# Performance work log

Measured on AMD Instinct MI355X. Metric: run time of the kernel, lower is better.

## Reference

```python
import jax, jax.numpy as jnp
import numpy as np
import math

N_HEAD = 12


def setup_inputs() -> dict:
    key = jax.random.key(0)
    ks = jax.random.split(key, 4)
    B, T, C = 8, 1024, 768
    s = 0.02
    return {
        "x": jax.random.normal(ks[0], (B, T, C), dtype=jnp.float32),
        "attn_mask": jnp.ones((B, T), dtype=jnp.int32),
        "W_attn": jax.random.normal(ks[1], (C, 3 * C), dtype=jnp.float32) * s,
        "b_attn": jnp.zeros((3 * C,), dtype=jnp.float32),
        "W_proj": jax.random.normal(ks[2], (C, C), dtype=jnp.float32) * s,
        "b_proj": jnp.zeros((C,), dtype=jnp.float32),
    }


def reference(x, attn_mask, W_attn, b_attn, W_proj, b_proj):
    B, T, C = x.shape
    hd = C // N_HEAD
    qkv = x @ W_attn + b_attn                      # [B, T, 3C]
    q, k, v = jnp.split(qkv, 3, axis=2)
    # [B, H, T, hd]
    q = q.reshape(B, T, N_HEAD, hd).transpose(0, 2, 1, 3)
    k = k.reshape(B, T, N_HEAD, hd).transpose(0, 2, 1, 3)
    v = v.reshape(B, T, N_HEAD, hd).transpose(0, 2, 1, 3)
    scores = jnp.einsum("bhqd,bhkd->bhqk", q, k) * (1.0 / math.sqrt(hd))
    mask = attn_mask[:, None, None, :]             # [B, 1, 1, T] broadcast over H, q
    scores = jnp.where(mask == 0, -jnp.inf, scores)
    attn = jax.nn.softmax(scores, axis=-1)
    out = jnp.einsum("bhqk,bhkd->bhqd", attn, v)   # [B, H, T, hd]
    out = out.transpose(0, 2, 1, 3).reshape(B, T, C)
    return out @ W_proj + b_proj
```

## Files before the change

### kernel.cpp

```cpp
#include <hip/hip_runtime.h>
#include <hip/hip_bf16.h>
#include <math.h>

constexpr int Bsz  = 8;
constexpr int Tseq = 1024;
constexpr int Cdim = 768;
constexpr int NH   = 12;
constexpr int HD   = 64;
constexpr int Mrows = Bsz * Tseq;
constexpr int C3    = 3 * Cdim;

using short8  = __attribute__((ext_vector_type(8))) short;
using s4v     = __attribute__((ext_vector_type(4))) short;
using floatx4 = __attribute__((ext_vector_type(4))) float;

__device__ __forceinline__ unsigned short f32_to_bf16_rn(float f) {
    unsigned int u = __float_as_uint(f);
    unsigned int r = u + 0x7FFFu + ((u >> 16) & 1u);
    return (unsigned short)(r >> 16);
}
__device__ __forceinline__ unsigned pack_bf16x2_rn(float a, float b) {
    float2 f2; f2.x = a; f2.y = b;
    __hip_bfloat162 h = __float22bfloat162_rn(f2);
    unsigned r;
    __builtin_memcpy(&r, &h, sizeof(r));
    return r;
}
__device__ __forceinline__ short8 lds_ld8(const unsigned short* p) {
    s4v a = *(const s4v*)p;
    s4v b = *(const s4v*)(p + 4);
    return __builtin_shufflevector(a, b, 0, 1, 2, 3, 4, 5, 6, 7);
}
__device__ __forceinline__ void lds_st8(unsigned short* p, short8 v) {
    *(s4v*)p       = __builtin_shufflevector(v, v, 0, 1, 2, 3);
    *(s4v*)(p + 4) = __builtin_shufflevector(v, v, 4, 5, 6, 7);
}

#define GLOAD_LDS16(g, l) __builtin_amdgcn_global_load_lds(                    \
    (const __attribute__((address_space(1))) void*)(g),                        \
    (__attribute__((address_space(3))) void*)(l), 16, 0, 0)

#define WAITVM0 asm volatile("s_waitcnt vmcnt(0)" ::: "memory")
#define LDS_XLANE_FENCE do {                                                   \
    asm volatile("s_waitcnt lgkmcnt(0)" ::: "memory");                         \
    __builtin_amdgcn_sched_barrier(0);                                         \
} while (0)

__global__ __launch_bounds__(256)
void to_bf16(const float* __restrict__ in, unsigned short* __restrict__ out, int n4)
{
    int t = blockIdx.x * blockDim.x + threadIdx.x;
    if (t >= n4) return;
    float4 v = ((const float4*)in)[t];
    ushort4 o;
    o.x = f32_to_bf16_rn(v.x);
    o.y = f32_to_bf16_rn(v.y);
    o.z = f32_to_bf16_rn(v.z);
    o.w = f32_to_bf16_rn(v.w);
    ((ushort4*)out)[t] = o;
}

__global__ __launch_bounds__(256)
void transpose_bf16(const float* __restrict__ in, unsigned short* __restrict__ out,
                    int K, int N)
{
    __shared__ float tile[32][33];
    const int k0 = blockIdx.y * 32, n0 = blockIdx.x * 32;
    const int tx = threadIdx.x & 31, ty = threadIdx.x >> 5;
    #pragma unroll
    for (int r = ty; r < 32; r += 8)
        tile[r][tx] = in[(size_t)(k0 + r) * N + n0 + tx];
    __syncthreads();
    #pragma unroll
    for (int r = ty; r < 32; r += 8)
        out[(size_t)(n0 + r) * K + k0 + tx] = f32_to_bf16_rn(tile[tx][r]);
}

template<int MH>
__device__ __forceinline__ void qkv_body(
    const unsigned short* __restrict__ A_g,
    const unsigned short* __restrict__ B_g,
    const float* __restrict__ bias,
    unsigned short* __restrict__ Cb,
    const int row0, const int col0, const int K, const int N,
    unsigned short* lds)
{
    constexpr int BK   = 32;
    constexpr int BUFS = 16384;

    const int tid  = threadIdx.x;
    const int wave = tid >> 6;
    const int lane = tid & 63;
    const int lm   = lane & 15;
    const int quad = lane >> 4;
    const int wy   = wave >> 2;
    const int wx   = wave & 3;
    const int NI   = K / BK;
    const int sq8  = (quad ^ ((lm ^ (lm >> 2)) & 3)) * 8;
    const int sr   = tid >> 2;
    const int sq   = tid & 3;

    floatx4 acc[4 * MH][4] = {};

    auto stageA = [&](int buf, int k0, int h) {
        const int r  = h * 128 + sr;
        const int gc = k0 + ((sq ^ ((r ^ (r >> 2)) & 3)) << 3);
        GLOAD_LDS16(A_g + (size_t)(row0 + r) * K + gc,
                    lds + buf * BUFS + r * 32 + sq * 8);
    };
    auto stageB = [&](int buf, int k0, int h) {
        const int r  = h * 128 + sr;
        const int gc = k0 + ((sq ^ ((r ^ (r >> 2)) & 3)) << 3);
        GLOAD_LDS16(B_g + (size_t)(col0 + r) * K + gc,
                    lds + buf * BUFS + 8192 + r * 32 + sq * 8);
    };

    #pragma unroll
    for (int h = 0; h < MH; ++h) stageA(0, 0, h);
    stageB(0, 0, 0); stageB(0, 0, 1);
    #pragma unroll
    for (int h = 0; h < MH; ++h) stageA(1, BK, h);
    stageB(1, BK, 0); stageB(1, BK, 1);
    if constexpr (MH == 2) asm volatile("s_waitcnt vmcnt(4)" ::: "memory");
    else                   asm volatile("s_waitcnt vmcnt(3)" ::: "memory");
    __builtin_amdgcn_s_barrier();

    short8 af[2 * MH], bf[4];
    int cur = 0;
    for (int kt = 0; kt < NI; ++kt) {
        const unsigned short* bufA = lds + cur * BUFS;
        const unsigned short* bufB = bufA + 8192;
        const int  stg  = (cur + 2 >= 3) ? cur - 1 : cur + 2;
        const int  k2   = (kt + 2) * BK;
        const bool doSt = (kt + 2 < NI);

        #pragma unroll
        for (int u = 0; u < 2 * MH; ++u)
            af[u] = *(const short8*)(bufA + (wy * (64 * MH) + u * 16 + lm) * 32 + sq8);
        #pragma unroll
        for (int j = 0; j < 4; ++j)
            bf[j] = *(const short8*)(bufB + (wx * 64 + j * 16 + lm) * 32 + sq8);
        if (doSt) {
            stageA(stg, k2, 0);
            if constexpr (MH == 2) stageA(stg, k2, 1); else stageB(stg, k2, 0);
        }
        __builtin_amdgcn_s_barrier();
        __builtin_amdgcn_s_setprio(1);
        #pragma unroll
        for (int u = 0; u < 2 * MH; ++u)
            #pragma unroll
            for (int j = 0; j < 4; ++j)
                acc[u][j] = __builtin_amdgcn_mfma_f32_16x16x32_bf16(af[u], bf[j], acc[u][j], 0, 0, 0);
        __builtin_amdgcn_s_setprio(0);
        __builtin_amdgcn_s_barrier();

        #pragma unroll
        for (int u = 0; u < 2 * MH; ++u)
            af[u] = *(const short8*)(bufA + (wy * (64 * MH) + (2 * MH + u) * 16 + lm) * 32 + sq8);
        if (doSt) {
            if constexpr (MH == 2) { stageB(stg, k2, 0); stageB(stg, k2, 1); }
            else                   stageB(stg, k2, 1);
        }
        __builtin_amdgcn_s_barrier();
        __builtin_amdgcn_s_setprio(1);
        #pragma unroll
        for (int u = 0; u < 2 * MH; ++u)
            #pragma unroll
            for (int j = 0; j < 4; ++j)
                acc[2 * MH + u][j] = __builtin_amdgcn_mfma_f32_16x16x32_bf16(af[u], bf[j], acc[2 * MH + u][j], 0, 0, 0);
        __builtin_amdgcn_s_setprio(0);
        if (kt == NI - 2) { WAITVM0; }
        else if (kt < NI - 2) {
            if constexpr (MH == 2) asm volatile("s_waitcnt vmcnt(4)" ::: "memory");
            else                   asm volatile("s_waitcnt vmcnt(3)" ::: "memory");
        }
        __builtin_amdgcn_s_barrier();

        cur = (cur == 2) ? 0 : cur + 1;
    }
    asm volatile("" ::: "memory");

    unsigned short* wbuf = lds + (NI % 3) * BUFS + wave * 1088;
    float bvj[4];
    #pragma unroll
    for (int j = 0; j < 4; ++j) bvj[j] = bias[col0 + wx * 64 + j * 16 + lm];
    #pragma unroll
    for (int i = 0; i < 4 * MH; ++i) {
        #pragma unroll
        for (int j = 0; j < 4; ++j) {
            #pragma unroll
            for (int r = 0; r < 4; ++r)
                wbuf[(quad * 4 + r) * 68 + j * 16 + lm] = f32_to_bf16_rn(acc[i][j][r] + bvj[j]);
        }
        asm volatile("s_waitcnt lgkmcnt(0)" ::: "memory");
        #pragma unroll
        for (int p = 0; p < 2; ++p) {
            const int lrow  = p * 8 + (lane >> 3);
            const int lcol8 = (lane & 7) * 8;
            short8 v = lds_ld8(&wbuf[lrow * 68 + lcol8]);
            *(short8*)(Cb + (size_t)(row0 + wy * (64 * MH) + i * 16 + lrow) * N +
                       col0 + wx * 64 + lcol8) = v;
        }
        asm volatile("s_waitcnt lgkmcnt(0)" ::: "memory");
    }
}

__global__ __launch_bounds__(512, 1)
void gemm_qkv8p(const unsigned short* __restrict__ A_g,
                const unsigned short* __restrict__ B_g,
                const float* __restrict__ bias,
                unsigned short* __restrict__ Cb)
{
    __shared__ __align__(16) unsigned short lds[3 * 16384];
    const int bid = blockIdx.x;
    if (bid < 256) {
        const int sid = (bid & 7) * 32 + (bid >> 3);
        qkv_body<2>(A_g, B_g, bias, Cb,
                    (sid >> 3) * 256, (sid & 7) * 256, Cdim, C3, lds);
    } else {
        const int t   = bid - 256;
        const int sid = (t & 7) * 8 + (t >> 3);
        qkv_body<1>(A_g, B_g, bias, Cb, sid * 128, 2048, Cdim, C3, lds);
    }
}

__global__ __launch_bounds__(256)
void gemm_proj(const unsigned short* __restrict__ AO_g,
               const unsigned short* __restrict__ B_g,
               const float* __restrict__ bias,
               float* __restrict__ C,
               int M, int N, int K)
{
    __shared__ __align__(16) unsigned short Ah[2][128 * 32];
    __shared__ __align__(16) unsigned short Bh[2][128 * 32];

    const int tid  = threadIdx.x;
    const int wave = tid >> 6;
    const int lane = tid & 63;
    const int lm   = lane & 15;
    const int quad = lane >> 4;
    const int wy   = wave >> 1, wx = wave & 1;
    const int row0 = blockIdx.y * 128;
    const int col0 = blockIdx.x * 128;

    const int sr  = lane >> 2;
    const int skp = (lane & 3) * 8;
    const int NI  = K / 32;

    floatx4 acc[4][4] = {};

    {
        const int head0 = skp >> 6, off0 = skp & 63;
        #pragma unroll
        for (int s = 0; s < 2; ++s) {
            const int r = (wave * 2 + s) * 16 + sr;
            GLOAD_LDS16(AO_g + (size_t)head0 * (Mrows * HD) + (size_t)(row0 + r) * HD + off0,
                        &Ah[0][r * 32 + skp]);
            GLOAD_LDS16(B_g + (size_t)(col0 + r) * K + skp, &Bh[0][r * 32 + skp]);
        }
    }
    __syncthreads();

    for (int kt = 0; kt < NI; ++kt) {
        const int cur = kt & 1, nxt = cur ^ 1;

        if (kt + 1 < NI) {
            const int k0   = (kt + 1) * 32;
            const int kk   = k0 + skp;
            const int head = kk >> 6;
            const int off  = kk & 63;
            #pragma unroll
            for (int s = 0; s < 2; ++s) {
                const int r = (wave * 2 + s) * 16 + sr;
                GLOAD_LDS16(AO_g + (size_t)head * (Mrows * HD) + (size_t)(row0 + r) * HD + off,
                            &Ah[nxt][r * 32 + skp]);
                GLOAD_LDS16(B_g + (size_t)(col0 + r) * K + k0 + skp, &Bh[nxt][r * 32 + skp]);
            }
        }

        short8 af[4];
        #pragma unroll
        for (int i = 0; i < 4; ++i)
            af[i] = *(const short8*)&Ah[cur][(wy * 64 + i * 16 + lm) * 32 + quad * 8];
        #pragma unroll
        for (int j = 0; j < 4; ++j) {
            short8 bfj = *(const short8*)&Bh[cur][(wx * 64 + j * 16 + lm) * 32 + quad * 8];
            #pragma unroll
            for (int i = 0; i < 4; ++i)
                acc[i][j] = __builtin_amdgcn_mfma_f32_16x16x32_bf16(af[i], bfj, acc[i][j], 0, 0, 0);
        }

        __syncthreads();
    }

    #pragma unroll
    for (int j = 0; j < 4; ++j) {
        const int col = col0 + wx * 64 + j * 16 + lm;
        const float bv = bias[col];
        #pragma unroll
        for (int i = 0; i < 4; ++i) {
            const int rowb = row0 + wy * 64 + i * 16 + quad * 4;
            #pragma unroll
            for (int r = 0; r < 4; ++r)
                C[(size_t)(rowb + r) * N + col] = acc[i][j][r] + bv;
        }
    }
}

__global__ __launch_bounds__(256, 2)
void attn_bf16(const unsigned short* __restrict__ qkv,
               const int* __restrict__ mask,
               unsigned short* __restrict__ outh)
{
    constexpr int LDW = 68;
    constexpr int NT  = Tseq / 64;
    __shared__ __align__(16) unsigned short Kh[2][64 * LDW];
    __shared__ __align__(16) unsigned short Vh[2][64 * LDW];
    __shared__ __align__(16) unsigned short Ph[128 * LDW];
    __shared__ float maskadd[2][64];
    __shared__ int   mflag[2];

    const int tid  = threadIdx.x;
    const int wave = tid >> 6;
    const int lane = tid & 63;
    const int lm   = lane & 15;
    const int quad = lane >> 4;
    const int idx  = blockIdx.x;
    const int bh   = idx % (Bsz * NH);
    const int qb   = idx / (Bsz * NH);
    const int b    = bh / NH;
    const int h    = bh % NH;
    const int q0   = qb * 128;
    const float scale = 0.125f;

    short8 qf[2][2];
    #pragma unroll
    for (int mt = 0; mt < 2; ++mt) {
        const size_t qrow = (size_t)(b * Tseq + q0 + wave * 32 + mt * 16 + lm) * C3 + h * HD;
        #pragma unroll
        for (int kf = 0; kf < 2; ++kf)
            qf[mt][kf] = *(const short8*)(qkv + qrow + kf * 32 + quad * 8);
    }

    const int sr0 = (tid & 31) * 2;
    const int sc  = (tid >> 5) * 8;

    short8 kh0, kh1, vh0, vh1;
    float  mreg = 0.f;

    {
        const size_t g0 = (size_t)(b * Tseq + sr0) * C3 + Cdim + h * HD + sc;
        kh0 = *(const short8*)(qkv + g0);
        kh1 = *(const short8*)(qkv + g0 + C3);
        vh0 = *(const short8*)(qkv + g0 + Cdim);
        vh1 = *(const short8*)(qkv + g0 + Cdim + C3);
        lds_st8(&Kh[0][sr0 * LDW + sc], kh0);
        lds_st8(&Kh[0][(sr0 + 1) * LDW + sc], kh1);
        #pragma unroll
        for (int i = 0; i < 8; ++i) {
            unsigned int pv = (unsigned int)(unsigned short)vh0[i] |
                              ((unsigned int)(unsigned short)vh1[i] << 16);
            *(unsigned int*)&Vh[0][(sc + i) * LDW + sr0] = pv;
        }
        if (tid < 64) {
            mreg = (mask[b * Tseq + tid] == 0) ? -1e30f : 0.0f;
            const int f = __all(mreg == 0.0f);
            maskadd[0][tid] = mreg;
            if (tid == 0) mflag[0] = f;
        }
    }
    __syncthreads();

    floatx4 O[2][4] = {};
    float lsum[2] = {0.f, 0.f};

    for (int kt = 0; kt < NT; ++kt) {
        const int cur = kt & 1;
        const int nxt = cur ^ 1;
        const unsigned short* Khc = Kh[cur];
        const unsigned short* Vhc = Vh[cur];

        if (kt + 1 < NT) {
            const size_t g0 = (size_t)(b * Tseq + (kt + 1) * 64 + sr0) * C3 + Cdim + h * HD + sc;
            kh0 = *(const short8*)(qkv + g0);
            kh1 = *(const short8*)(qkv + g0 + C3);
            vh0 = *(const short8*)(qkv + g0 + Cdim);
            vh1 = *(const short8*)(qkv + g0 + Cdim + C3);
            if (tid < 64) mreg = (mask[b * Tseq + (kt + 1) * 64 + tid] == 0) ? -1e30f : 0.0f;
        }

        floatx4 S[2][4] = {};
        #pragma unroll
        for (int kf = 0; kf < 2; ++kf) {
            short8 kh[4];
            #pragma unroll
            for (int nt = 0; nt < 4; ++nt)
                kh[nt] = lds_ld8(&Khc[(nt * 16 + lm) * LDW + kf * 32 + quad * 8]);
            #pragma unroll
            for (int mt = 0; mt < 2; ++mt)
                #pragma unroll
                for (int nt = 0; nt < 4; ++nt)
                    S[mt][nt] = __builtin_amdgcn_mfma_f32_16x16x32_bf16(kh[nt], qf[mt][kf], S[mt][nt], 0, 0, 0);
        }

        const int nomask = mflag[cur];

        if (nomask) {
            #pragma unroll
            for (int mt = 0; mt < 2; ++mt) {
                const int prow = (wave * 32 + mt * 16 + lm) * LDW;
                #pragma unroll
                for (int nt = 0; nt < 4; ++nt) {
                    float p0 = __expf(S[mt][nt][0] * scale);
                    float p1 = __expf(S[mt][nt][1] * scale);
                    float p2 = __expf(S[mt][nt][2] * scale);
                    float p3 = __expf(S[mt][nt][3] * scale);
                    lsum[mt] += p0; lsum[mt] += p1;
                    lsum[mt] += p2; lsum[mt] += p3;
                    uint2 pk2;
                    pk2.x = pack_bf16x2_rn(p0, p1);
                    pk2.y = pack_bf16x2_rn(p2, p3);
                    *(uint2*)&Ph[prow + nt * 16 + quad * 4] = pk2;
                }
            }
        } else {
            float madd[4][4];
            #pragma unroll
            for (int nt = 0; nt < 4; ++nt)
                #pragma unroll
                for (int r = 0; r < 4; ++r)
                    madd[nt][r] = maskadd[cur][nt * 16 + quad * 4 + r];
            #pragma unroll
            for (int mt = 0; mt < 2; ++mt) {
                const int prow = (wave * 32 + mt * 16 + lm) * LDW;
                #pragma unroll
                for (int nt = 0; nt < 4; ++nt) {
                    float p0 = __expf(S[mt][nt][0] * scale + madd[nt][0]);
                    float p1 = __expf(S[mt][nt][1] * scale + madd[nt][1]);
                    float p2 = __expf(S[mt][nt][2] * scale + madd[nt][2]);
                    float p3 = __expf(S[mt][nt][3] * scale + madd[nt][3]);
                    lsum[mt] += p0; lsum[mt] += p1;
                    lsum[mt] += p2; lsum[mt] += p3;
                    uint2 pk2;
                    pk2.x = pack_bf16x2_rn(p0, p1);
                    pk2.y = pack_bf16x2_rn(p2, p3);
                    *(uint2*)&Ph[prow + nt * 16 + quad * 4] = pk2;
                }
            }
        }

        LDS_XLANE_FENCE;

        #pragma unroll
        for (int kf = 0; kf < 2; ++kf) {
            short8 pf[2];
            #pragma unroll
            for (int mt = 0; mt < 2; ++mt)
                pf[mt] = lds_ld8(&Ph[(wave * 32 + mt * 16 + lm) * LDW + kf * 32 + quad * 8]);
            #pragma unroll
            for (int dt = 0; dt < 4; ++dt) {
                short8 vh = lds_ld8(&Vhc[(dt * 16 + lm) * LDW + kf * 32 + quad * 8]);
                #pragma unroll
                for (int mt = 0; mt < 2; ++mt)
                    O[mt][dt] = __builtin_amdgcn_mfma_f32_16x16x32_bf16(vh, pf[mt], O[mt][dt], 0, 0, 0);
            }
        }

        if (kt + 1 < NT) {
            lds_st8(&Kh[nxt][sr0 * LDW + sc], kh0);
            lds_st8(&Kh[nxt][(sr0 + 1) * LDW + sc], kh1);
            #pragma unroll
            for (int i = 0; i < 8; ++i) {
                unsigned int pv = (unsigned int)(unsigned short)vh0[i] |
                                  ((unsigned int)(unsigned short)vh1[i] << 16);
                *(unsigned int*)&Vh[nxt][(sc + i) * LDW + sr0] = pv;
            }
            if (tid < 64) {
                const int f = __all(mreg == 0.0f);
                maskadd[nxt][tid] = mreg;
                if (tid == 0) mflag[nxt] = f;
            }
        }
        __syncthreads();
    }

    #pragma unroll
    for (int mt = 0; mt < 2; ++mt) {
        lsum[mt] += __shfl_xor(lsum[mt], 16);
        lsum[mt] += __shfl_xor(lsum[mt], 32);
        const float inv_l = 1.0f / lsum[mt];
        const size_t row = (size_t)h * (Mrows * HD) +
                           (size_t)(b * Tseq + q0 + wave * 32 + mt * 16 + lm) * HD;
        #pragma unroll
        for (int dt = 0; dt < 4; ++dt) {
            ushort4 hv;
            unsigned short* hp = &hv.x;
            #pragma unroll
            for (int r = 0; r < 4; ++r)
                hp[r] = f32_to_bf16_rn(O[mt][dt][r] * inv_l);
            *(ushort4*)(outh + row + dt * 16 + quad * 4) = hv;
        }
    }
}

extern "C" void kernel_launch(void* const* d_in, const int* in_sizes, int n_in,
                              void* d_out, int out_size, void* d_ws, size_t ws_size,
                              hipStream_t stream)
{
    const float* x      = (const float*)d_in[0];
    const int*   mask   = (const int*)  d_in[1];
    const float* W_attn = (const float*)d_in[2];
    const float* b_attn = (const float*)d_in[3];
    const float* W_proj = (const float*)d_in[4];
    const float* b_proj = (const float*)d_in[5];
    float* out = (float*)d_out;

    unsigned short* xh    = (unsigned short*)d_ws;
    unsigned short* wat_h = xh    + (size_t)Mrows * Cdim;
    unsigned short* wpt_h = wat_h + (size_t)C3 * Cdim;
    unsigned short* qkvh  = wpt_h + (size_t)Cdim * Cdim;
    unsigned short* aoh   = xh;

    dim3 blk(256);

    to_bf16<<<dim3(Mrows * Cdim / 4 / 256), blk, 0, stream>>>(x, xh, Mrows * Cdim / 4);
    transpose_bf16<<<dim3(C3 / 32, Cdim / 32), blk, 0, stream>>>(W_attn, wat_h, Cdim, C3);
    transpose_bf16<<<dim3(Cdim / 32, Cdim / 32), blk, 0, stream>>>(W_proj, wpt_h, Cdim, Cdim);

    gemm_qkv8p<<<dim3(320), dim3(512), 0, stream>>>(xh, wat_h, b_attn, qkvh);

    attn_bf16<<<dim3((Tseq / 128) * Bsz * NH), blk, 0, stream>>>(qkvh, mask, aoh);

    gemm_proj<<<dim3(Cdim / 128, Mrows / 128), blk, 0, stream>>>(
        aoh, wpt_h, b_proj, out, Mrows, Cdim, Cdim);
}
```

Baseline: 205.9 us.

## Keep attention probabilities in registers via lane shuffles instead of LDS round-trip

The softmax probabilities P are no longer written to and re-read from a shared-memory tile. They stay in registers, and a cross-lane shuffle rearranges them into the operand layout the PV MFMA needs. To make this work, the K rows and the mask entries are stored in LDS under a bit-swizzled key permutation, so the S accumulator layout lines up with the shuffled P fragments. Dropping the P tile frees LDS, and launch bounds are raised to request 3 blocks per CU, which may increase register pressure.

```diff
diff --git a/kernel.cpp b/kernel.cpp
--- a/kernel.cpp
+++ b/kernel.cpp
@@ -13,6 +13,7 @@
 using short8  = __attribute__((ext_vector_type(8))) short;
 using s4v     = __attribute__((ext_vector_type(4))) short;
 using floatx4 = __attribute__((ext_vector_type(4))) float;
+using uintx4  = __attribute__((ext_vector_type(4))) unsigned int;
 
 __device__ __forceinline__ unsigned short f32_to_bf16_rn(float f) {
     unsigned int u = __float_as_uint(f);
@@ -41,10 +42,6 @@
     (__attribute__((address_space(3))) void*)(l), 16, 0, 0)
 
 #define WAITVM0 asm volatile("s_waitcnt vmcnt(0)" ::: "memory")
-#define LDS_XLANE_FENCE do {                                                   \
-    asm volatile("s_waitcnt lgkmcnt(0)" ::: "memory");                         \
-    __builtin_amdgcn_sched_barrier(0);                                         \
-} while (0)
 
 __global__ __launch_bounds__(256)
 void to_bf16(const float* __restrict__ in, unsigned short* __restrict__ out, int n4)
@@ -307,7 +304,7 @@
     }
 }
 
-__global__ __launch_bounds__(256, 2)
+__global__ __launch_bounds__(256, 3)
 void attn_bf16(const unsigned short* __restrict__ qkv,
                const int* __restrict__ mask,
                unsigned short* __restrict__ outh)
@@ -316,7 +313,6 @@
     constexpr int NT  = Tseq / 64;
     __shared__ __align__(16) unsigned short Kh[2][64 * LDW];
     __shared__ __align__(16) unsigned short Vh[2][64 * LDW];
-    __shared__ __align__(16) unsigned short Ph[128 * LDW];
     __shared__ float maskadd[2][64];
     __shared__ int   mflag[2];
 
@@ -342,30 +338,32 @@
             qf[mt][kf] = *(const short8*)(qkv + qrow + kf * 32 + quad * 8);
     }
 
-    const int sr0 = (tid & 31) * 2;
+    const int tr0 = (tid & 31) * 2;
     const int sc  = (tid >> 5) * 8;
+    const int ps0 = (tr0 & 0x27) | ((tr0 & 0x10) >> 1) | ((tr0 & 0x08) << 1);
+    const int smi = (tid & 0x27) | ((tid & 0x10) >> 1) | ((tid & 0x08) << 1);
 
     short8 kh0, kh1, vh0, vh1;
     float  mreg = 0.f;
 
     {
-        const size_t g0 = (size_t)(b * Tseq + sr0) * C3 + Cdim + h * HD + sc;
+        const size_t g0 = (size_t)(b * Tseq + tr0) * C3 + Cdim + h * HD + sc;
         kh0 = *(const short8*)(qkv + g0);
         kh1 = *(const short8*)(qkv + g0 + C3);
         vh0 = *(const short8*)(qkv + g0 + Cdim);
         vh1 = *(const short8*)(qkv + g0 + Cdim + C3);
-        lds_st8(&Kh[0][sr0 * LDW + sc], kh0);
-        lds_st8(&Kh[0][(sr0 + 1) * LDW + sc], kh1);
+        lds_st8(&Kh[0][ps0 * LDW + sc], kh0);
+        lds_st8(&Kh[0][(ps0 + 1) * LDW + sc], kh1);
         #pragma unroll
         for (int i = 0; i < 8; ++i) {
             unsigned int pv = (unsigned int)(unsigned short)vh0[i] |
                               ((unsigned int)(unsigned short)vh1[i] << 16);
-            *(unsigned int*)&Vh[0][(sc + i) * LDW + sr0] = pv;
+            *(unsigned int*)&Vh[0][(sc + i) * LDW + tr0] = pv;
         }
         if (tid < 64) {
             mreg = (mask[b * Tseq + tid] == 0) ? -1e30f : 0.0f;
             const int f = __all(mreg == 0.0f);
-            maskadd[0][tid] = mreg;
+            maskadd[0][smi] = mreg;
             if (tid == 0) mflag[0] = f;
         }
     }
@@ -381,7 +379,7 @@
         const unsigned short* Vhc = Vh[cur];
 
         if (kt + 1 < NT) {
-            const size_t g0 = (size_t)(b * Tseq + (kt + 1) * 64 + sr0) * C3 + Cdim + h * HD + sc;
+            const size_t g0 = (size_t)(b * Tseq + (kt + 1) * 64 + tr0) * C3 + Cdim + h * HD + sc;
             kh0 = *(const short8*)(qkv + g0);
             kh1 = *(const short8*)(qkv + g0 + C3);
             vh0 = *(const short8*)(qkv + g0 + Cdim);
@@ -405,10 +403,10 @@
 
         const int nomask = mflag[cur];
 
+        unsigned X[2][8];
         if (nomask) {
             #pragma unroll
             for (int mt = 0; mt < 2; ++mt) {
-                const int prow = (wave * 32 + mt * 16 + lm) * LDW;
                 #pragma unroll
                 for (int nt = 0; nt < 4; ++nt) {
                     float p0 = __expf(S[mt][nt][0] * scale);
@@ -417,10 +415,8 @@
                     float p3 = __expf(S[mt][nt][3] * scale);
                     lsum[mt] += p0; lsum[mt] += p1;
                     lsum[mt] += p2; lsum[mt] += p3;
-                    uint2 pk2;
-                    pk2.x = pack_bf16x2_rn(p0, p1);
-                    pk2.y = pack_bf16x2_rn(p2, p3);
-                    *(uint2*)&Ph[prow + nt * 16 + quad * 4] = pk2;
+                    X[mt][nt * 2 + 0] = pack_bf16x2_rn(p0, p1);
+                    X[mt][nt * 2 + 1] = pack_bf16x2_rn(p2, p3);
                 }
             }
         } else {
@@ -432,7 +428,6 @@
                     madd[nt][r] = maskadd[cur][nt * 16 + quad * 4 + r];
             #pragma unroll
             for (int mt = 0; mt < 2; ++mt) {
-                const int prow = (wave * 32 + mt * 16 + lm) * LDW;
                 #pragma unroll
                 for (int nt = 0; nt < 4; ++nt) {
                     float p0 = __expf(S[mt][nt][0] * scale + madd[nt][0]);
@@ -441,43 +436,54 @@
                     float p3 = __expf(S[mt][nt][3] * scale + madd[nt][3]);
                     lsum[mt] += p0; lsum[mt] += p1;
                     lsum[mt] += p2; lsum[mt] += p3;
-                    uint2 pk2;
-                    pk2.x = pack_bf16x2_rn(p0, p1);
-                    pk2.y = pack_bf16x2_rn(p2, p3);
-                    *(uint2*)&Ph[prow + nt * 16 + quad * 4] = pk2;
+                    X[mt][nt * 2 + 0] = pack_bf16x2_rn(p0, p1);
+                    X[mt][nt * 2 + 1] = pack_bf16x2_rn(p2, p3);
                 }
             }
         }
 
-        LDS_XLANE_FENCE;
+        const bool qodd = (quad & 1);
+        short8 pf[2][2];
+        #pragma unroll
+        for (int mt = 0; mt < 2; ++mt) {
+            #pragma unroll
+            for (int pr = 0; pr < 4; ++pr) {
+                const int a  = (pr & 1) | ((pr & 2) << 1);
+                const int b2 = a + 2;
+                unsigned t = qodd ? X[mt][a] : X[mt][b2];
+                t = (unsigned)__shfl_xor((int)t, 16);
+                X[mt][a]  = qodd ? t : X[mt][a];
+                X[mt][b2] = qodd ? X[mt][b2] : t;
+            }
+            uintx4 u0 = {X[mt][0], X[mt][1], X[mt][2], X[mt][3]};
+            uintx4 u1 = {X[mt][4], X[mt][5], X[mt][6], X[mt][7]};
+            __builtin_memcpy(&pf[mt][0], &u0, 16);
+            __builtin_memcpy(&pf[mt][1], &u1, 16);
+        }
 
         #pragma unroll
         for (int kf = 0; kf < 2; ++kf) {
-            short8 pf[2];
-            #pragma unroll
-            for (int mt = 0; mt < 2; ++mt)
-                pf[mt] = lds_ld8(&Ph[(wave * 32 + mt * 16 + lm) * LDW + kf * 32 + quad * 8]);
             #pragma unroll
             for (int dt = 0; dt < 4; ++dt) {
                 short8 vh = lds_ld8(&Vhc[(dt * 16 + lm) * LDW + kf * 32 + quad * 8]);
                 #pragma unroll
                 for (int mt = 0; mt < 2; ++mt)
-                    O[mt][dt] = __builtin_amdgcn_mfma_f32_16x16x32_bf16(vh, pf[mt], O[mt][dt], 0, 0, 0);
+                    O[mt][dt] = __builtin_amdgcn_mfma_f32_16x16x32_bf16(vh, pf[mt][kf], O[mt][dt], 0, 0, 0);
             }
         }
 
         if (kt + 1 < NT) {
-            lds_st8(&Kh[nxt][sr0 * LDW + sc], kh0);
-            lds_st8(&Kh[nxt][(sr0 + 1) * LDW + sc], kh1);
+            lds_st8(&Kh[nxt][ps0 * LDW + sc], kh0);
+            lds_st8(&Kh[nxt][(ps0 + 1) * LDW + sc], kh1);
             #pragma unroll
             for (int i = 0; i < 8; ++i) {
                 unsigned int pv = (unsigned int)(unsigned short)vh0[i] |
                                   ((unsigned int)(unsigned short)vh1[i] << 16);
-                *(unsigned int*)&Vh[nxt][(sc + i) * LDW + sr0] = pv;
+                *(unsigned int*)&Vh[nxt][(sc + i) * LDW + tr0] = pv;
             }
             if (tid < 64) {
                 const int f = __all(mreg == 0.0f);
-                maskadd[nxt][tid] = mreg;
+                maskadd[nxt][smi] = mreg;
                 if (tid == 0) mflag[nxt] = f;
             }
         }
```

New measurement: 208.2 us. About the same (+1.1%).
